# Optimization experiments

Measured on AMD Instinct MI355X. Metric: run time of the kernel, lower is better.

## Reference

```python
import jax, jax.numpy as jnp
import numpy as np

CVOCAB = 600  # static extended-vocab size (torch code uses max(src_map)+1; src_map values < 600)


def setup_inputs() -> dict:
    key = jax.random.key(0)
    k1, k2, k3, k4, k5 = jax.random.split(key, 5)
    N, D, V = 2048, 1024, 50257  # N = batch*tlen
    B, S = 32, 400               # batch, source length
    return {
        "hidden": jax.random.normal(k1, (N, D), jnp.float32),
        "orig_prob": jax.random.normal(k2, (N, V), jnp.float32),
        "attn": jax.random.uniform(k3, (N, S), jnp.float32),
        "src_map": jax.random.randint(k4, (B, S), 0, CVOCAB, jnp.int32),
        "W_copy": jax.random.normal(k5, (1, D), jnp.float32) * 0.02,
        "b_copy": jnp.zeros((1,), jnp.float32),
    }


def reference(hidden, orig_prob, attn, src_map, W_copy, b_copy):
    batch, slen = src_map.shape
    # p_softmax over target vocab
    prob = jax.nn.softmax(orig_prob, axis=1)                  # (N, V)
    # copy switch p(z=1)
    p_copy = jax.nn.sigmoid(hidden @ W_copy.T + b_copy)       # (N, 1)
    out_prob = prob * (1.0 - p_copy)                          # (N, V)
    mul_attn = (attn * p_copy).reshape(batch, -1, slen)       # (B, T, S)

    # one-hot + bmm in the original == scatter-add of attention mass into extended vocab slots
    def scatter_batch(a, sm):
        # a: (T, S), sm: (S,) -> (T, CVOCAB), duplicates accumulate
        return jnp.zeros((a.shape[0], CVOCAB), a.dtype).at[:, sm].add(a)

    copy_prob = jax.vmap(scatter_batch)(mul_attn, src_map)    # (B, T, CVOCAB)
    return out_prob, copy_prob.reshape(-1, CVOCAB)
```

## Files before the change

kernel.cpp:

```cpp
#include <hip/hip_runtime.h>
#include <math.h>

#define WAVE 64
#define BDIM 1024
#define NIT  13

typedef float f32x4 __attribute__((ext_vector_type(4)));

__global__ __launch_bounds__(BDIM, 4) void fused_kernel(
        const float* __restrict__ x,
        const float* __restrict__ hidden,
        const float* __restrict__ W,
        const float* __restrict__ bptr,
        const float* __restrict__ attn,
        const int*   __restrict__ src_map,
        float* __restrict__ out_prob,
        float* __restrict__ copy_out,
        int V, int D, int S, int C, int T) {
    const int row  = blockIdx.x;
    const int tid  = threadIdx.x;
    const int lane = tid & (WAVE - 1);
    const int wid  = tid / WAVE;

    __shared__ float red_sum[BDIM / WAVE];
    __shared__ float red_dot[BDIM / WAVE];
    __shared__ float bcast[2];
    extern __shared__ float bins[];

    for (int j = tid; j < C; j += BDIM) bins[j] = 0.f;

    const float* xr = x + (size_t)row * V;
    float v[NIT * 4];
    float lsum = 0.f;
    #pragma unroll
    for (int i = 0; i < NIT; ++i) {
        int e = (i * BDIM + tid) * 4;
        if (e + 3 < V) {
            float4 t = *(const float4*)(xr + e);
            v[4*i+0] = t.x; v[4*i+1] = t.y; v[4*i+2] = t.z; v[4*i+3] = t.w;
        } else {
            #pragma unroll
            for (int k = 0; k < 4; ++k)
                v[4*i+k] = (e + k < V) ? xr[e + k] : -INFINITY;
        }
    }
    #pragma unroll
    for (int j = 0; j < NIT * 4; ++j) {
        v[j] = __expf(v[j]);
        lsum += v[j];
    }

    float ldot = 0.f;
    {
        const float* h = hidden + (size_t)row * D;
        for (int e = tid; e < D; e += BDIM)
            ldot += h[e] * W[e];
    }

    #pragma unroll
    for (int off = 32; off >= 1; off >>= 1) {
        lsum += __shfl_xor(lsum, off, WAVE);
        ldot += __shfl_xor(ldot, off, WAVE);
    }
    if (lane == 0) { red_sum[wid] = lsum; red_dot[wid] = ldot; }
    __syncthreads();
    if (tid == 0) {
        float s = 0.f, dd = 0.f;
        #pragma unroll
        for (int w = 0; w < BDIM / WAVE; ++w) { s += red_sum[w]; dd += red_dot[w]; }
        float pc = 1.f / (1.f + __expf(-(dd + bptr[0])));
        bcast[0] = (1.f - pc) / s;
        bcast[1] = pc;
    }
    __syncthreads();
    const float scale = bcast[0];
    const float pc    = bcast[1];

    float* outr = out_prob + (size_t)row * V;
    #pragma unroll
    for (int i = 0; i < NIT; ++i) {
        int e = (i * BDIM + tid) * 4;
        if (e + 3 < V) {
            f32x4 o;
            o.x = v[4*i+0] * scale; o.y = v[4*i+1] * scale;
            o.z = v[4*i+2] * scale; o.w = v[4*i+3] * scale;
            __builtin_nontemporal_store(o, (f32x4*)(outr + e));
        } else {
            #pragma unroll
            for (int k = 0; k < 4; ++k)
                if (e + k < V) outr[e + k] = v[4*i+k] * scale;
        }
    }

    {
        const float* ar = attn + (size_t)row * S;
        const int*   sm = src_map + (size_t)(row / T) * S;
        for (int s = tid; s < S; s += BDIM)
            atomicAdd(&bins[sm[s]], ar[s] * pc);
        __syncthreads();
        float* outc = copy_out + (size_t)row * C;
        for (int j = tid; j < C; j += BDIM)
            outc[j] = bins[j];
    }
}

extern "C" void kernel_launch(void* const* d_in, const int* in_sizes, int n_in,
                              void* d_out, int out_size, void* d_ws, size_t ws_size,
                              hipStream_t stream) {
    const float* hidden  = (const float*)d_in[0];
    const float* orig    = (const float*)d_in[1];
    const float* attn    = (const float*)d_in[2];
    const int*   src_map = (const int*)  d_in[3];
    const float* W       = (const float*)d_in[4];
    const float* b       = (const float*)d_in[5];

    const int D = in_sizes[4];
    const int N = in_sizes[0] / D;
    const int V = in_sizes[1] / N;
    const int S = in_sizes[2] / N;
    const int B = in_sizes[3] / S;
    const int T = N / B;
    const int C = out_size / N - V;

    float* out_prob = (float*)d_out;
    float* copy_out = (float*)d_out + (size_t)N * V;

    fused_kernel<<<N, BDIM, C * sizeof(float), stream>>>(
        orig, hidden, W, b, attn, src_map, out_prob, copy_out, V, D, S, C, T);
}
```

Baseline: 181.6 us.

## Make kernel persistent over row chunks and prefetch next row during stores

Launches a fixed grid of 256 blocks, each processing a contiguous chunk of rows instead of one block per row. While writing the scaled softmax output of the current row, each thread loads the next row's logits into registers, overlapping reads with writes. This removes per-block launch and ramp-up costs but cuts resident parallelism to one 1024-thread block per CU slot, relying on manual prefetch to keep memory busy. It risks lower occupancy and more memory-level serialization than the many-block version.

```diff
diff --git a/kernel.cpp b/kernel.cpp
--- a/kernel.cpp
+++ b/kernel.cpp
@@ -4,6 +4,7 @@
 #define WAVE 64
 #define BDIM 1024
 #define NIT  13
+#define GRID 256
 
 typedef float f32x4 __attribute__((ext_vector_type(4)));
 
@@ -16,8 +17,7 @@
         const int*   __restrict__ src_map,
         float* __restrict__ out_prob,
         float* __restrict__ copy_out,
-        int V, int D, int S, int C, int T) {
-    const int row  = blockIdx.x;
+        int N, int V, int D, int S, int C, int T) {
     const int tid  = threadIdx.x;
     const int lane = tid & (WAVE - 1);
     const int wid  = tid / WAVE;
@@ -27,80 +27,101 @@
     __shared__ float bcast[2];
     extern __shared__ float bins[];
 
-    for (int j = tid; j < C; j += BDIM) bins[j] = 0.f;
+    const int rpb = (N + GRID - 1) / GRID;
+    const int rb  = blockIdx.x * rpb;
+    const float bias = bptr[0];
 
-    const float* xr = x + (size_t)row * V;
     float v[NIT * 4];
-    float lsum = 0.f;
-    #pragma unroll
-    for (int i = 0; i < NIT; ++i) {
-        int e = (i * BDIM + tid) * 4;
-        if (e + 3 < V) {
-            float4 t = *(const float4*)(xr + e);
-            v[4*i+0] = t.x; v[4*i+1] = t.y; v[4*i+2] = t.z; v[4*i+3] = t.w;
-        } else {
-            #pragma unroll
-            for (int k = 0; k < 4; ++k)
-                v[4*i+k] = (e + k < V) ? xr[e + k] : -INFINITY;
-        }
-    }
-    #pragma unroll
-    for (int j = 0; j < NIT * 4; ++j) {
-        v[j] = __expf(v[j]);
-        lsum += v[j];
-    }
 
-    float ldot = 0.f;
-    {
-        const float* h = hidden + (size_t)row * D;
-        for (int e = tid; e < D; e += BDIM)
-            ldot += h[e] * W[e];
-    }
-
-    #pragma unroll
-    for (int off = 32; off >= 1; off >>= 1) {
-        lsum += __shfl_xor(lsum, off, WAVE);
-        ldot += __shfl_xor(ldot, off, WAVE);
-    }
-    if (lane == 0) { red_sum[wid] = lsum; red_dot[wid] = ldot; }
-    __syncthreads();
-    if (tid == 0) {
-        float s = 0.f, dd = 0.f;
+    if (rb < N) {
+        const float* xr = x + (size_t)rb * V;
         #pragma unroll
-        for (int w = 0; w < BDIM / WAVE; ++w) { s += red_sum[w]; dd += red_dot[w]; }
-        float pc = 1.f / (1.f + __expf(-(dd + bptr[0])));
-        bcast[0] = (1.f - pc) / s;
-        bcast[1] = pc;
-    }
-    __syncthreads();
-    const float scale = bcast[0];
-    const float pc    = bcast[1];
-
-    float* outr = out_prob + (size_t)row * V;
-    #pragma unroll
-    for (int i = 0; i < NIT; ++i) {
-        int e = (i * BDIM + tid) * 4;
-        if (e + 3 < V) {
-            f32x4 o;
-            o.x = v[4*i+0] * scale; o.y = v[4*i+1] * scale;
-            o.z = v[4*i+2] * scale; o.w = v[4*i+3] * scale;
-            __builtin_nontemporal_store(o, (f32x4*)(outr + e));
-        } else {
-            #pragma unroll
-            for (int k = 0; k < 4; ++k)
-                if (e + k < V) outr[e + k] = v[4*i+k] * scale;
+        for (int i = 0; i < NIT; ++i) {
+            int e = (i * BDIM + tid) * 4;
+            if (e + 3 < V) {
+                float4 t = *(const float4*)(xr + e);
+                v[4*i+0] = t.x; v[4*i+1] = t.y; v[4*i+2] = t.z; v[4*i+3] = t.w;
+            } else {
+                #pragma unroll
+                for (int k = 0; k < 4; ++k)
+                    v[4*i+k] = (e + k < V) ? xr[e + k] : -INFINITY;
+            }
         }
     }
 
-    {
-        const float* ar = attn + (size_t)row * S;
-        const int*   sm = src_map + (size_t)(row / T) * S;
-        for (int s = tid; s < S; s += BDIM)
-            atomicAdd(&bins[sm[s]], ar[s] * pc);
+    for (int k = 0; k < rpb; ++k) {
+        const int row = rb + k;
+        if (row >= N) break;
+
+        for (int j = tid; j < C; j += BDIM) bins[j] = 0.f;
+
+        float lsum = 0.f;
+        #pragma unroll
+        for (int j = 0; j < NIT * 4; ++j) {
+            v[j] = __expf(v[j]);
+            lsum += v[j];
+        }
+
+        float ldot = 0.f;
+        {
+            const float* h = hidden + (size_t)row * D;
+            for (int e = tid; e < D; e += BDIM)
+                ldot += h[e] * W[e];
+        }
+
+        #pragma unroll
+        for (int off = 32; off >= 1; off >>= 1) {
+            lsum += __shfl_xor(lsum, off, WAVE);
+            ldot += __shfl_xor(ldot, off, WAVE);
+        }
+        if (lane == 0) { red_sum[wid] = lsum; red_dot[wid] = ldot; }
         __syncthreads();
-        float* outc = copy_out + (size_t)row * C;
-        for (int j = tid; j < C; j += BDIM)
-            outc[j] = bins[j];
+        if (tid == 0) {
+            float s = 0.f, dd = 0.f;
+            #pragma unroll
+            for (int w = 0; w < BDIM / WAVE; ++w) { s += red_sum[w]; dd += red_dot[w]; }
+            float pc = 1.f / (1.f + __expf(-(dd + bias)));
+            bcast[0] = (1.f - pc) / s;
+            bcast[1] = pc;
+        }
+        __syncthreads();
+        const float scale = bcast[0];
+        const float pc    = bcast[1];
+
+        float* outr = out_prob + (size_t)row * V;
+        const float* xn = x + (size_t)(row + 1) * V;
+        const bool more = (k + 1 < rpb) && (row + 1 < N);
+        #pragma unroll
+        for (int i = 0; i < NIT; ++i) {
+            int e = (i * BDIM + tid) * 4;
+            if (e + 3 < V) {
+                f32x4 o;
+                o.x = v[4*i+0] * scale; o.y = v[4*i+1] * scale;
+                o.z = v[4*i+2] * scale; o.w = v[4*i+3] * scale;
+                __builtin_nontemporal_store(o, (f32x4*)(outr + e));
+                if (more) {
+                    float4 t = *(const float4*)(xn + e);
+                    v[4*i+0] = t.x; v[4*i+1] = t.y; v[4*i+2] = t.z; v[4*i+3] = t.w;
+                }
+            } else {
+                #pragma unroll
+                for (int kk = 0; kk < 4; ++kk) {
+                    if (e + kk < V) outr[e + kk] = v[4*i+kk] * scale;
+                    if (more) v[4*i+kk] = (e + kk < V) ? xn[e + kk] : -INFINITY;
+                }
+            }
+        }
+
+        {
+            const float* ar = attn + (size_t)row * S;
+            const int*   sm = src_map + (size_t)(row / T) * S;
+            for (int s = tid; s < S; s += BDIM)
+                atomicAdd(&bins[sm[s]], ar[s] * pc);
+            __syncthreads();
+            float* outc = copy_out + (size_t)row * C;
+            for (int j = tid; j < C; j += BDIM)
+                outc[j] = bins[j];
+        }
     }
 }
 
@@ -125,6 +146,6 @@
     float* out_prob = (float*)d_out;
     float* copy_out = (float*)d_out + (size_t)N * V;
 
-    fused_kernel<<<N, BDIM, C * sizeof(float), stream>>>(
-        orig, hidden, W, b, attn, src_map, out_prob, copy_out, V, D, S, C, T);
+    fused_kernel<<<GRID, BDIM, C * sizeof(float), stream>>>(
+        orig, hidden, W, b, attn, src_map, out_prob, copy_out, N, V, D, S, C, T);
 }
```

Result: slower. 194.5 us (+7.1%).
